# Optimization experiments

Hardware: AMD Instinct MI355X
Metric: run time of the kernel (lower is better)

The kernel has to match this reference:

```python
import jax, jax.numpy as jnp
import numpy as np

NUM_CLASSES = 6

def _weight_matrix(num_classes, weight_type='quadratic'):
    i = jnp.arange(num_classes, dtype=jnp.float32)
    d = jnp.abs(i[:, None] - i[None, :])
    if weight_type == 'linear':
        return d
    elif weight_type == 'quadratic':
        return d ** 2
    else:
        raise ValueError("weight_type must be 'linear' or 'quadratic'")

def setup_inputs() -> dict:
    key = jax.random.key(0)
    k1, k2 = jax.random.split(key)
    N = 4_000_000
    y_pred = jax.random.normal(k1, (N, NUM_CLASSES), dtype=jnp.float32)
    y_true = jax.random.randint(k2, (N,), 0, NUM_CLASSES, dtype=jnp.int64)
    return {"y_pred": y_pred, "y_true": y_true}

def reference(y_pred, y_true):
    C = NUM_CLASSES
    t = y_true.reshape(-1).astype(jnp.int32)
    probs = jax.nn.softmax(y_pred, axis=1)
    p = jnp.argmax(probs, axis=1).astype(jnp.int32)
    # histograms over classes (equivalent to torch.histc with bins=C, min=0, max=C-1)
    hist_true = jnp.bincount(t, length=C).astype(jnp.float32)
    hist_pred = jnp.bincount(p, length=C).astype(jnp.float32)
    # confusion matrix in one fused scatter-add pass (replaces the Python loop)
    flat = t * C + p  # [N]
    confusion = jnp.bincount(flat, length=C * C).astype(jnp.float32).reshape(C, C)
    confusion = confusion / confusion.sum()
    expected = jnp.outer(hist_true, hist_pred)
    expected = expected / expected.sum()
    W = _weight_matrix(C, 'quadratic')
    kappa = 1.0 - (W * confusion).sum() / (W * expected).sum()
    return kappa
```

## Files before the change

### kernel.cpp

```cpp
#include <hip/hip_runtime.h>


#define NC 6
#define NBINS 36
#define BLOCK 256
#define WPB (BLOCK / 64)
#define GRID 1024
#define SEGS 16
#define FIN_THREADS (NBINS * SEGS)

typedef float f4 __attribute__((ext_vector_type(4)));

__global__ __launch_bounds__(BLOCK) void kappa_count(
    const f4* __restrict__ yp4, const unsigned long long* __restrict__ yt2,
    const float* __restrict__ yp, const int* __restrict__ yt,
    unsigned int* __restrict__ gconf, int npairs, int N) {
    __shared__ unsigned int sconf[WPB][NBINS];
    const int tid = threadIdx.x;
    const int w = tid >> 6;
    if (tid < WPB * NBINS) ((unsigned int*)sconf)[tid] = 0u;
    __syncthreads();

    unsigned int* my = sconf[w];
    const int stride = GRID * BLOCK;

    for (int i = blockIdx.x * BLOCK + tid; i < npairs; i += stride) {
        const f4 a = __builtin_nontemporal_load(&yp4[3 * i]);
        const f4 b = __builtin_nontemporal_load(&yp4[3 * i + 1]);
        const f4 d = __builtin_nontemporal_load(&yp4[3 * i + 2]);
        const unsigned long long tt = __builtin_nontemporal_load(&yt2[i]);
        const int t0 = (int)(tt & 0xffffffffull);
        const int t1 = (int)(tt >> 32);

        float m = a.x; int p = 0;
        if (a.y > m) { m = a.y; p = 1; }
        if (a.z > m) { m = a.z; p = 2; }
        if (a.w > m) { m = a.w; p = 3; }
        if (b.x > m) { m = b.x; p = 4; }
        if (b.y > m) { m = b.y; p = 5; }
        atomicAdd(&my[t0 * NC + p], 1u);

        m = b.z; p = 0;
        if (b.w > m) { m = b.w; p = 1; }
        if (d.x > m) { m = d.x; p = 2; }
        if (d.y > m) { m = d.y; p = 3; }
        if (d.z > m) { m = d.z; p = 4; }
        if (d.w > m) { m = d.w; p = 5; }
        atomicAdd(&my[t1 * NC + p], 1u);
    }

    if ((N & 1) && blockIdx.x == 0 && tid == 0) {
        const int r = N - 1;
        float m = yp[r * NC]; int p = 0;
        #pragma unroll
        for (int j = 1; j < NC; ++j) {
            const float v = yp[r * NC + j];
            if (v > m) { m = v; p = j; }
        }
        atomicAdd(&my[yt[r] * NC + p], 1u);
    }

    __syncthreads();
    if (tid < NBINS) {
        unsigned int s = 0;
        #pragma unroll
        for (int k = 0; k < WPB; ++k) s += sconf[k][tid];
        gconf[blockIdx.x * NBINS + tid] = s;
    }
}

__global__ void kappa_final_kernel(const unsigned int* __restrict__ gconf,
                                   float* __restrict__ out, long long N) {
    __shared__ unsigned int part[SEGS][NBINS];
    __shared__ unsigned int conf_s[NBINS];
    const int tid = threadIdx.x;
    if (tid < FIN_THREADS) {
        const int bin = tid % NBINS;
        const int seg = tid / NBINS;
        unsigned int s = 0;
        const int b0 = seg * (GRID / SEGS);
        #pragma unroll 8
        for (int b = b0; b < b0 + GRID / SEGS; ++b) s += gconf[b * NBINS + bin];
        part[seg][bin] = s;
    }
    __syncthreads();
    if (tid < NBINS) {
        unsigned int tot = 0;
        #pragma unroll
        for (int s2 = 0; s2 < SEGS; ++s2) tot += part[s2][tid];
        conf_s[tid] = tot;
    }
    __syncthreads();
    if (tid == 0) {
        long long conf[NBINS], ht[NC], hp[NC];
        #pragma unroll
        for (int i = 0; i < NC; ++i) { ht[i] = 0; hp[i] = 0; }
        #pragma unroll
        for (int k = 0; k < NBINS; ++k) conf[k] = (long long)conf_s[k];

        long long num = 0;
        #pragma unroll
        for (int i = 0; i < NC; ++i)
            #pragma unroll
            for (int j = 0; j < NC; ++j) {
                const long long w = (long long)(i - j) * (i - j);
                num += w * conf[i * NC + j];
                ht[i] += conf[i * NC + j];
                hp[j] += conf[i * NC + j];
            }
        long long den = 0;
        #pragma unroll
        for (int i = 0; i < NC; ++i)
            #pragma unroll
            for (int j = 0; j < NC; ++j)
                den += (long long)(i - j) * (i - j) * ht[i] * hp[j];

        out[0] = (float)(1.0 - ((double)num * (double)N) / (double)den);
    }
}

extern "C" void kernel_launch(void* const* d_in, const int* in_sizes, int n_in,
                              void* d_out, int out_size, void* d_ws, size_t ws_size,
                              hipStream_t stream) {
    const float* yp = (const float*)d_in[0];
    const int* yt = (const int*)d_in[1];
    const int N = in_sizes[1];
    unsigned int* gconf = (unsigned int*)d_ws;

    const int npairs = N / 2;
    kappa_count<<<GRID, BLOCK, 0, stream>>>(
        (const f4*)yp, (const unsigned long long*)yt, yp, yt, gconf, npairs, N);
    kappa_final_kernel<<<1, FIN_THREADS, 0, stream>>>(gconf, (float*)d_out,
                                                      (long long)N);
}
```

Measured before the change: 148.8 us.

## Coalesce per-wave chunk loads and transpose through LDS staging

Each wave now loads a contiguous 64-pair chunk with fully coalesced dwordx4 loads, using inline asm with sc1 nt streaming hints. It writes the chunk to LDS and reads it back transposed, so each lane gets its own 6-float rows. A separate tail path handles pairs left over after whole chunks. The aim is to replace the strided per-thread 48-byte loads with coalesced ones, at the cost of LDS traffic and a full vmcnt wait that serializes memory and compute within each wave.

```diff
diff --git a/kernel.cpp b/kernel.cpp
--- a/kernel.cpp
+++ b/kernel.cpp
@@ -6,29 +6,57 @@
 #define BLOCK 256
 #define WPB (BLOCK / 64)
 #define GRID 1024
+#define CHUNK 64
 #define SEGS 16
 #define FIN_THREADS (NBINS * SEGS)
 
 typedef float f4 __attribute__((ext_vector_type(4)));
 
+__device__ __forceinline__ f4 ld_stream_b128(const f4* p) {
+    f4 r;
+    asm volatile("global_load_dwordx4 %0, %1, off sc1 nt"
+                 : "=v"(r) : "v"(p) : "memory");
+    return r;
+}
+__device__ __forceinline__ unsigned long long ld_stream_b64(
+    const unsigned long long* p) {
+    unsigned long long r;
+    asm volatile("global_load_dwordx2 %0, %1, off sc1 nt"
+                 : "=v"(r) : "v"(p) : "memory");
+    return r;
+}
+
 __global__ __launch_bounds__(BLOCK) void kappa_count(
     const f4* __restrict__ yp4, const unsigned long long* __restrict__ yt2,
     const float* __restrict__ yp, const int* __restrict__ yt,
     unsigned int* __restrict__ gconf, int npairs, int N) {
+    __shared__ f4 stage[WPB][3 * CHUNK];
     __shared__ unsigned int sconf[WPB][NBINS];
     const int tid = threadIdx.x;
     const int w = tid >> 6;
+    const int L = tid & 63;
     if (tid < WPB * NBINS) ((unsigned int*)sconf)[tid] = 0u;
     __syncthreads();
 
     unsigned int* my = sconf[w];
-    const int stride = GRID * BLOCK;
+    f4* st = stage[w];
 
-    for (int i = blockIdx.x * BLOCK + tid; i < npairs; i += stride) {
-        const f4 a = __builtin_nontemporal_load(&yp4[3 * i]);
-        const f4 b = __builtin_nontemporal_load(&yp4[3 * i + 1]);
-        const f4 d = __builtin_nontemporal_load(&yp4[3 * i + 2]);
-        const unsigned long long tt = __builtin_nontemporal_load(&yt2[i]);
+    const int nchunks = npairs / CHUNK;
+    const int gwaves = GRID * WPB;
+    for (int c = blockIdx.x * WPB + w; c < nchunks; c += gwaves) {
+        const f4 g0 = ld_stream_b128(&yp4[c * 3 * CHUNK + L]);
+        const f4 g1 = ld_stream_b128(&yp4[c * 3 * CHUNK + 64 + L]);
+        const f4 g2 = ld_stream_b128(&yp4[c * 3 * CHUNK + 128 + L]);
+        const unsigned long long tt = ld_stream_b64(&yt2[c * CHUNK + L]);
+        asm volatile("s_waitcnt vmcnt(0)" ::: "memory");
+        __builtin_amdgcn_sched_barrier(0);
+        st[L] = g0;
+        st[64 + L] = g1;
+        st[128 + L] = g2;
+        __threadfence_block();
+        const f4 a = st[3 * L];
+        const f4 b = st[3 * L + 1];
+        const f4 d = st[3 * L + 2];
         const int t0 = (int)(tt & 0xffffffffull);
         const int t1 = (int)(tt >> 32);
 
@@ -40,6 +68,31 @@
         if (b.y > m) { m = b.y; p = 5; }
         atomicAdd(&my[t0 * NC + p], 1u);
 
+        m = b.z; p = 0;
+        if (b.w > m) { m = b.w; p = 1; }
+        if (d.x > m) { m = d.x; p = 2; }
+        if (d.y > m) { m = d.y; p = 3; }
+        if (d.z > m) { m = d.z; p = 4; }
+        if (d.w > m) { m = d.w; p = 5; }
+        atomicAdd(&my[t1 * NC + p], 1u);
+    }
+
+    const int rem0 = nchunks * CHUNK;
+    if (blockIdx.x == 0 && tid < npairs - rem0) {
+        const int i = rem0 + tid;
+        const f4 a = yp4[3 * i];
+        const f4 b = yp4[3 * i + 1];
+        const f4 d = yp4[3 * i + 2];
+        const unsigned long long tt = yt2[i];
+        const int t0 = (int)(tt & 0xffffffffull);
+        const int t1 = (int)(tt >> 32);
+        float m = a.x; int p = 0;
+        if (a.y > m) { m = a.y; p = 1; }
+        if (a.z > m) { m = a.z; p = 2; }
+        if (a.w > m) { m = a.w; p = 3; }
+        if (b.x > m) { m = b.x; p = 4; }
+        if (b.y > m) { m = b.y; p = 5; }
+        atomicAdd(&my[t0 * NC + p], 1u);
         m = b.z; p = 0;
         if (b.w > m) { m = b.w; p = 1; }
         if (d.x > m) { m = d.x; p = 2; }
```

Result: faster. 145.0 us (median of 2 runs) (-2.6%).
